# Optimization experiments

Measured on AMD Instinct MI355X. Metric: run time of the kernel, lower is better.

## Reference

```python
import jax, jax.numpy as jnp
import numpy as np

# Static sizes: S scenes of P pedestrians each; B = S*P total peds.
S, P, HD, ED, GH, GO, MD, T = 128, 32, 32, 16, 72, 8, 64, 8
B = S * P


def setup_inputs() -> dict:
    key = jax.random.key(0)
    ks = jax.random.split(key, 24)
    f32 = jnp.float32
    inp = {
        'last_pos': jax.random.normal(ks[0], (B, 2), f32),
        'last_pos_rel': jax.random.normal(ks[1], (B, 2), f32),
        'hh': jax.random.normal(ks[2], (B, HD), f32),
        'ch': jax.random.normal(ks[3], (B, HD), f32),
        # uniform scenes: [start, end) pairs
        'seq_start_end': jnp.stack([jnp.arange(S) * P, (jnp.arange(S) + 1) * P], axis=1).astype(jnp.int64),
        'end_group': jax.random.randint(ks[4], (B, 1), 0, 5, jnp.int32),
        # decoder spatial embedding Linear(2, ED)
        'W_se': jax.random.normal(ks[5], (2, ED), f32) * 0.5,
        'b_se': jax.random.normal(ks[6], (ED,), f32) * 0.05,
        # LSTM (num_layers=1), torch gate order i,f,g,o
        'Wih': jax.random.normal(ks[7], (4 * HD, ED), f32) * 0.15,
        'Whh': jax.random.normal(ks[8], (4 * HD, HD), f32) * 0.15,
        'bih': jax.random.normal(ks[9], (4 * HD,), f32) * 0.05,
        'bhh': jax.random.normal(ks[10], (4 * HD,), f32) * 0.05,
        # hidden2pos Linear(HD, 2)
        'W_hp': jax.random.normal(ks[11], (HD, 2), f32) * 0.15,
        'b_hp': jax.random.normal(ks[12], (2,), f32) * 0.05,
        # pooling spatial embedding Linear(2, ED)
        'W_pse': jax.random.normal(ks[13], (2, ED), f32) * 0.5,
        'b_pse': jax.random.normal(ks[14], (ED,), f32) * 0.05,
        # intra-group GCN weights (48->72->8)
        'W1a': jax.random.normal(ks[15], (ED + HD, GH), f32) * 0.05,
        'W2a': jax.random.normal(ks[16], (GH, GO), f32) * 0.05,
        # inter-group GCN weights
        'W1b': jax.random.normal(ks[17], (ED + HD, GH), f32) * 0.05,
        'W2b': jax.random.normal(ks[18], (GH, GO), f32) * 0.05,
        # mlp: (HD + 2*GO) -> MD -> HD, relu after each layer
        'W_m1': jax.random.normal(ks[19], (HD + 2 * GO, MD), f32) * 0.15,
        'b_m1': jax.random.normal(ks[20], (MD,), f32) * 0.05,
        'W_m2': jax.random.normal(ks[21], (MD, HD), f32) * 0.15,
        'b_m2': jax.random.normal(ks[22], (HD,), f32) * 0.05,
    }
    return inp


def _pool(h, pos, g, W_pse, b_pse, W1a, W2a, W1b, W2b):
    # h: [B,HD] hidden, pos: [B,2] current positions, g: [B] int group labels
    hid = h.reshape(S, P, HD)
    ps = pos.reshape(S, P, 2)
    gg = g.reshape(S, P)
    # rel[s,i,j] = pos[j] - pos[i]  (matches curr_end_pos_1 - curr_end_pos_2)
    rel = ps[:, None, :, :] - ps[:, :, None, :]
    emb = rel @ W_pse + b_pse                                     # [S,P,P,ED]
    X = jnp.concatenate([emb, jnp.broadcast_to(hid[:, None], (S, P, P, HD))], -1)
    e = jnp.eye(P, dtype=bool)
    # adj_all[i,j,k] = (j==k) | (i==j) | (i==k)
    adj_all = (e[None, :, :] | e[:, :, None] | e[:, None, :]).astype(X.dtype)
    same = ((gg[:, :, None] == gg[:, None, :]) & (gg[:, :, None] != 0)) | e[None]
    diff = (~same) | e[None]

    def norm(adj):
        # faithful to the original normalize(): divide adj[s,i,j,k] by sum_k adj[s,j,i,k]
        denom = jnp.sum(adj, axis=3)                               # [S,i,j]
        return adj / jnp.swapaxes(denom, 1, 2)[..., None]

    A_s = norm(adj_all[None] * same[:, None].astype(X.dtype))      # [S,P,P,P]
    A_d = norm(adj_all[None] * diff[:, None].astype(X.dtype))

    def gcn(A, H, W1, W2):
        H = jax.nn.relu(jnp.einsum('sijk,sikd->sijd', A, H) @ W1)
        H = jax.nn.relu(jnp.einsum('sijk,sikd->sijd', A, H) @ W2)
        return H

    feat = jnp.concatenate([gcn(A_s, X, W1a, W2a), gcn(A_d, X, W1b, W2b)], -1)  # [S,P,P,2*GO]
    return jnp.max(feat, axis=2).reshape(B, 2 * GO)


def reference(last_pos, last_pos_rel, hh, ch, seq_start_end, end_group,
              W_se, b_se, Wih, Whh, bih, bhh, W_hp, b_hp, W_pse, b_pse,
              W1a, W2a, W1b, W2b, W_m1, b_m1, W_m2, b_m2):
    g = end_group.reshape(-1)
    dec_in = last_pos_rel @ W_se + b_se

    def step(carry, _):
        h, c, lp, x = carry
        gates = x @ Wih.T + bih + h @ Whh.T + bhh
        i, f, gc, o = jnp.split(gates, 4, axis=-1)
        c2 = jax.nn.sigmoid(f) * c + jax.nn.sigmoid(i) * jnp.tanh(gc)
        h2 = jax.nn.sigmoid(o) * jnp.tanh(c2)
        rel_pos = h2 @ W_hp + b_hp
        cur = rel_pos + lp
        ph = _pool(h2, cur, g, W_pse, b_pse, W1a, W2a, W1b, W2b)
        dh = jax.nn.relu(jnp.concatenate([h2, ph], -1) @ W_m1 + b_m1)
        dh = jax.nn.relu(dh @ W_m2 + b_m2)
        x2 = rel_pos @ W_se + b_se
        return (dh, c2, cur, x2), rel_pos

    _, rels = jax.lax.scan(step, (hh, ch, last_pos, dec_in), None, length=T)
    return rels  # pred_traj_fake_rel: [T, B, 2]
```

## Files before the change

kernel.cpp:

```cpp
#include <hip/hip_runtime.h>

#define NS 128
#define NP 32
#define HD 32
#define ED 16
#define GH 72
#define GO 8
#define MD 64
#define TT 8
#define NB (NS*NP)
#define EW 76

#define SLOT 272
#define WS_NEED (256*2*SLOT*4)

typedef float v2f __attribute__((ext_vector_type(2)));

__device__ __forceinline__ float sigm(float x){ return 1.0f/(1.0f+__expf(-x)); }
__device__ __forceinline__ float tanhfast(float x){ return 1.0f - 2.0f/(__expf(2.0f*x)+1.0f); }
__device__ __forceinline__ unsigned rne16(float f){
  unsigned u = __float_as_uint(f);
  u += 0x7fffu + ((u>>16)&1u);
  return u>>16;
}
__device__ __forceinline__ float lo16(unsigned v){ return __uint_as_float(v<<16); }
__device__ __forceinline__ float hi16(unsigned v){ return __uint_as_float(v & 0xffff0000u); }
__device__ __forceinline__ float rdlane(float v, int l){
  return __int_as_float(__builtin_amdgcn_readlane(__float_as_int(v), l));
}
template<int C>
__device__ __forceinline__ float dppx(float x){
  return __int_as_float(__builtin_amdgcn_update_dpp(0, __float_as_int(x), C, 0xF, 0xF, true));
}
#define XOR1 0xB1
#define XOR2 0x4E

__global__ __launch_bounds__(1024, 1) void decoder_kernel_split(
    const float* __restrict__ last_pos, const float* __restrict__ last_pos_rel,
    const float* __restrict__ hh, const float* __restrict__ ch,
    const int*  __restrict__ eg,
    const float* __restrict__ W_se, const float* __restrict__ b_se,
    const float* __restrict__ Wih, const float* __restrict__ Whh,
    const float* __restrict__ bih, const float* __restrict__ bhh,
    const float* __restrict__ W_hp, const float* __restrict__ b_hp,
    const float* __restrict__ W_pse, const float* __restrict__ b_pse,
    const float* __restrict__ W1a, const float* __restrict__ W2a,
    const float* __restrict__ W1b, const float* __restrict__ W2b,
    const float* __restrict__ W_m1, const float* __restrict__ b_m1,
    const float* __restrict__ W_m2, const float* __restrict__ b_m2,
    float* __restrict__ out, float* __restrict__ ws)
{
  const int tid   = threadIdx.x;
  const int scn   = blockIdx.x >> 1;
  const int myM   = blockIdx.x & 1;
  const int lane  = tid & 31;
  const int grp32 = tid >> 5;

  __shared__ __align__(16) float uni[4096];
  __shared__ __align__(16) unsigned W1pT[GH][16];
  __shared__ __align__(16) float Wp1[2][GH];
  __shared__ __align__(16) float c1l[GH];
  __shared__ __align__(16) float ebuf[NP*EW];
  __shared__ __align__(16) float hbuf[NP][HD];
  __shared__ __align__(16) float h2buf[NP][36];
  __shared__ __align__(16) float GS[5][GH];
  __shared__ __align__(16) float phbuf[NP][16];
  __shared__ __align__(16) unsigned Wm1p[48][32];
  __shared__ __align__(16) unsigned Wm2p[32][32];
  __shared__ float lpbuf[NP][2], rpbuf[NP][2], Whp[HD][2];
  __shared__ float bm1l[MD], bm2l[HD], bhp2[2];
  __shared__ unsigned bm[NP];
  __shared__ unsigned gmsk[5];
  __shared__ float invn[NP];
  __shared__ int gl[NP];

  float* const a1 = uni;

  const int mybase = (scn*2 + myM)*2;
  const int pbase  = (scn*2 + 1 - myM)*2;

  const int myrow = tid & 127;
  const int pq4   = tid >> 7;
  float wrow[HD];
  #pragma unroll
  for (int c = 0; c < HD/4; c++) {
    float4 w = *(const float4*)(Whh + myrow*HD + c*4);
    wrow[c*4+0]=w.x; wrow[c*4+1]=w.y; wrow[c*4+2]=w.z; wrow[c*4+3]=w.w;
  }
  float wf0 = 0.f, wf1 = 0.f, bfr = bih[myrow] + bhh[myrow];
  #pragma unroll
  for (int e = 0; e < ED; e++) {
    float wv = Wih[myrow*ED + e];
    wf0 = fmaf(W_se[e],    wv, wf0);
    wf1 = fmaf(W_se[ED+e], wv, wf1);
    bfr = fmaf(b_se[e],    wv, bfr);
  }

  float creg = ch[(scn*NP + grp32)*HD + lane];
  hbuf[grp32][lane] = hh[(scn*NP + grp32)*HD + lane];

  if (tid < NP) {
    int gi = eg[scn*NP + tid];
    gl[tid] = gi;
    unsigned sm = 0;
    for (int j = 0; j < NP; j++) {
      int gj = eg[scn*NP + j];
      bool sj = (j == tid) || (gi == gj && gi != 0);
      sm |= ((unsigned)sj) << j;
    }
    unsigned mk = myM ? ((~sm) | (1u << tid)) : sm;
    bm[tid] = mk;
    invn[tid] = 1.0f/(float)__popc(mk);
  }
  if (tid < 5) {
    unsigned mv = 0;
    for (int j = 0; j < NP; j++) if (eg[scn*NP + j] == tid) mv |= (1u << j);
    gmsk[tid] = (tid == 0) ? 0xFFFFFFFFu : mv;
  }
  if (tid < 64) {
    int p = tid >> 1, k = tid & 1;
    lpbuf[p][k] = last_pos[(scn*NP+p)*2+k];
    rpbuf[p][k] = last_pos_rel[(scn*NP+p)*2+k];
    Whp[p][k]   = W_hp[tid];
    bm1l[tid]   = b_m1[tid];
  }
  if (tid < 32) bm2l[tid] = b_m2[tid];
  if (tid < 2)  bhp2[tid] = b_hp[tid];
  const float* W1my = myM ? W1b : W1a;
  const float* W2g  = myM ? W2b : W2a;
  if (tid < GH) {
    int d = tid;
    float s0 = 0.f, s1 = 0.f, sc1 = 0.f;
    for (int e = 0; e < ED; e++) {
      float w = W1my[e*GH + d];
      s0  += W_pse[e]    * w;
      s1  += W_pse[ED+e] * w;
      sc1 += b_pse[e]    * w;
    }
    Wp1[0][d] = s0; Wp1[1][d] = s1; c1l[d] = sc1;
  }
  #pragma unroll
  for (int r = 0; r < 2; r++) {
    int u = tid + 1024*r;
    if (u < 16*GH) {
      int k2 = u/GH, d = u%GH;
      unsigned lo = rne16(W1my[(ED+2*k2  )*GH + d]);
      unsigned hi = rne16(W1my[(ED+2*k2+1)*GH + d]);
      W1pT[d][k2] = lo | (hi << 16);
    }
  }
  #pragma unroll
  for (int r = 0; r < 2; r++) {
    int u = tid + 1024*r;
    if (u < 1536) {
      int k = u >> 5, uu = u & 31;
      Wm1p[k][uu] = rne16(W_m1[k*MD + uu]) | (rne16(W_m1[k*MD + 32 + uu]) << 16);
    }
  }
  {
    int k = tid >> 5, uu = tid & 31;
    Wm2p[k][uu] = rne16(W_m2[k*HD + uu]) | (rne16(W_m2[(k+32)*HD + uu]) << 16);
  }
  __syncthreads();

  for (int t = 0; t < TT; t++) {
    {
      float hv[4];
      #pragma unroll
      for (int pp2 = 0; pp2 < 4; pp2++) hv[pp2] = hbuf[pq4*4 + pp2][lane];
      float rG[4];
      #pragma unroll
      for (int pp2 = 0; pp2 < 4; pp2++) {
        int p = pq4*4 + pp2;
        float acc = fmaf(rpbuf[p][0], wf0, fmaf(rpbuf[p][1], wf1, bfr));
        #pragma unroll
        for (int c = 0; c < HD; c++)
          acc = fmaf(rdlane(hv[pp2], c), wrow[c], acc);
        rG[pp2] = acc;
      }
      #pragma unroll
      for (int pp2 = 0; pp2 < 4; pp2++) uni[(pq4*4+pp2)*128 + myrow] = rG[pp2];
    }
    __syncthreads();

    {
      int p = grp32, n = lane;
      float gi_ = uni[p*128 +       n];
      float gf_ = uni[p*128 +  32 + n];
      float gg_ = uni[p*128 +  64 + n];
      float go_ = uni[p*128 +  96 + n];
      float c2 = sigm(gf_)*creg + sigm(gi_)*tanhfast(gg_);
      creg = c2;
      float h2 = sigm(go_)*tanhfast(c2);
      h2buf[p][n] = h2;
      float r0 = h2 * Whp[n][0];
      float r1 = h2 * Whp[n][1];
      r0 += dppx<XOR1>(r0); r1 += dppx<XOR1>(r1);
      r0 += dppx<XOR2>(r0); r1 += dppx<XOR2>(r1);
      #pragma unroll
      for (int off = 4; off < 32; off <<= 1) {
        r0 += __shfl_xor(r0, off, 32);
        r1 += __shfl_xor(r1, off, 32);
      }
      r0 += bhp2[0]; r1 += bhp2[1];
      if (n == 0) {
        if (myM == 0) {
          out[t*NB*2 + (scn*NP+p)*2 + 0] = r0;
          out[t*NB*2 + (scn*NP+p)*2 + 1] = r1;
        }
        rpbuf[p][0] = r0;  rpbuf[p][1] = r1;
        lpbuf[p][0] += r0; lpbuf[p][1] += r1;
      }
    }
    __syncthreads();

    {
      const int j = lane;
      float lpj0 = lpbuf[j][0], lpj1 = lpbuf[j][1];
      float h2row[HD];
      #pragma unroll
      for (int c = 0; c < 8; c++) {
        float4 v = *(const float4*)&h2buf[j][c*4];
        h2row[c*4+0]=v.x; h2row[c*4+1]=v.y; h2row[c*4+2]=v.z; h2row[c*4+3]=v.w;
      }
      #pragma unroll
      for (int r = 0; r < 3; r++) {
        int d = grp32 + 32*r;
        if (d < GH) {
          float av = fmaf(lpj0, Wp1[0][d], lpj1*Wp1[1][d]);
          #pragma unroll
          for (int k8 = 0; k8 < 4; k8++) {
            uint4 w4 = *(const uint4*)&W1pT[d][k8*4];
            av = fmaf(h2row[k8*8+0], lo16(w4.x), av);
            av = fmaf(h2row[k8*8+1], hi16(w4.x), av);
            av = fmaf(h2row[k8*8+2], lo16(w4.y), av);
            av = fmaf(h2row[k8*8+3], hi16(w4.y), av);
            av = fmaf(h2row[k8*8+4], lo16(w4.z), av);
            av = fmaf(h2row[k8*8+5], hi16(w4.z), av);
            av = fmaf(h2row[k8*8+6], lo16(w4.w), av);
            av = fmaf(h2row[k8*8+7], hi16(w4.w), av);
          }
          a1[j*EW + d] = av;
        }
      }
      #pragma unroll
      for (int ii = 0; ii < 3; ii++) {
        int idx = tid + 1024*ii;
        if (idx < NP*GH) {
          int d = idx >> 5, i2 = idx & 31;
          ebuf[i2*EW + d] = fmaf(-lpbuf[i2][1], Wp1[1][d],
                            fmaf(-lpbuf[i2][0], Wp1[0][d], c1l[d]));
        }
      }
    }
    __syncthreads();

    if (tid < 5*GH) {
      int g = tid / GH, d = tid - g*GH;
      unsigned gmv = gmsk[g];
      float tot = 0.f, sg = 0.f;
      #pragma unroll
      for (int j2 = 0; j2 < NP; j2++) {
        float av = a1[j2*EW + d];
        tot += av;
        sg  += ((gmv >> j2) & 1u) ? av : 0.f;
      }
      GS[g][d] = myM ? ((g == 0) ? tot : tot - sg)
                     : ((g == 0) ? tot : sg);
    }
    __syncthreads();

    {
      const int j = lane, i = grp32;
      unsigned bmv = bm[i];
      bool mij = (bmv >> j) & 1u;
      bool diag = (j == i);
      int gi = gl[i];
      float in_ = invn[i];
      const float *p0, *p1; float c0, c1c;
      if (diag) {
        if (myM == 0) { p0 = gi ? &GS[gi][0] : (a1 + i*EW); c0 = in_; p1 = a1 + i*EW; c1c = 0.f; }
        else          { p0 = &GS[gi][0];                    c0 = in_; p1 = a1 + i*EW; c1c = gi ? in_ : 0.f; }
      } else if (mij) { p0 = a1 + j*EW; c0 = 0.5f; p1 = a1 + i*EW; c1c = 0.5f; }
      else            { p0 = a1 + j*EW; c0 = 1.0f; p1 = a1 + j*EW; c1c = 0.f; }
      const float* erow = ebuf + i*EW;
      v2f qv[4];
      #pragma unroll
      for (int h = 0; h < 4; h++) qv[h] = (v2f){0.f, 0.f};
      for (int d4 = 0; d4 < GH/4; d4++) {
        float4 e4 = *(const float4*)(erow + d4*4);
        float4 va = diag ? *(const float4*)(p0 + d4*4)
                         : *(const float4*)(a1 + j*EW + d4*4);
        float4 vb = *(const float4*)(p1 + d4*4);
        float tv[4];
        tv[0] = fmaxf(fmaf(c0, va.x, fmaf(c1c, vb.x, e4.x)), 0.f);
        tv[1] = fmaxf(fmaf(c0, va.y, fmaf(c1c, vb.y, e4.y)), 0.f);
        tv[2] = fmaxf(fmaf(c0, va.z, fmaf(c1c, vb.z, e4.z)), 0.f);
        tv[3] = fmaxf(fmaf(c0, va.w, fmaf(c1c, vb.w, e4.w)), 0.f);
        #pragma unroll
        for (int k = 0; k < 4; k++) {
          const float* wr = W2g + (d4*4+k)*GO;
          v2f wA = {wr[0], wr[1]}, wB = {wr[2], wr[3]};
          v2f wC = {wr[4], wr[5]}, wD = {wr[6], wr[7]};
          v2f tk = {tv[k], tv[k]};
          qv[0] += tk*wA; qv[1] += tk*wB; qv[2] += tk*wC; qv[3] += tk*wD;
        }
      }
      float q[8];
      #pragma unroll
      for (int h = 0; h < 4; h++) { q[2*h] = qv[h][0]; q[2*h+1] = qv[h][1]; }
      float sq[8];
      #pragma unroll
      for (int o = 0; o < 8; o++) sq[o] = mij ? q[o] : 0.f;
      #pragma unroll
      for (int o = 0; o < 8; o++) sq[o] += dppx<XOR1>(sq[o]);
      #pragma unroll
      for (int o = 0; o < 8; o++) sq[o] += dppx<XOR2>(sq[o]);
      #pragma unroll
      for (int off = 4; off < 32; off <<= 1) {
        #pragma unroll
        for (int o = 0; o < 8; o++) sq[o] += __shfl_xor(sq[o], off, 32);
      }
      float qd[8];
      #pragma unroll
      for (int o = 0; o < 8; o++) qd[o] = __shfl(q[o], i, 32);
      float F[8];
      if (diag) {
        #pragma unroll
        for (int o = 0; o < 8; o++) F[o] = fmaxf(sq[o]*in_, 0.f);
      } else {
        float scl = mij ? 0.5f : 1.0f;
        #pragma unroll
        for (int o = 0; o < 8; o++)
          F[o] = fmaxf((q[o] + (mij ? qd[o] : 0.f))*scl, 0.f);
      }
      #pragma unroll
      for (int o = 0; o < 8; o++) F[o] = fmaxf(F[o], dppx<XOR1>(F[o]));
      #pragma unroll
      for (int o = 0; o < 8; o++) F[o] = fmaxf(F[o], dppx<XOR2>(F[o]));
      #pragma unroll
      for (int off = 4; off < 32; off <<= 1) {
        #pragma unroll
        for (int o = 0; o < 8; o++) F[o] = fmaxf(F[o], __shfl_xor(F[o], off, 32));
      }
      if (j == 0) {
        const int slw = (mybase + (t & 1))*SLOT;
        #pragma unroll
        for (int o = 0; o < 8; o++) {
          phbuf[i][myM*GO + o] = F[o];
          atomicExch(ws + slw + i*8 + o, F[o]);
        }
      }
    }
    __syncthreads();

    const int sl  = (mybase + (t & 1))*SLOT;
    const int psl = (pbase  + (t & 1))*SLOT;
    if (tid == 0) atomicExch((unsigned*)(ws + sl + 256), (unsigned)(t + 1));
    asm volatile("" ::: "memory");
    const int p4 = grp32, u4 = lane;
    float m1lo = bm1l[u4], m1hi = bm1l[32 + u4];
    {
      #pragma unroll
      for (int c = 0; c < 8; c++) {
        float4 v = *(const float4*)&h2buf[p4][c*4];
        unsigned w0 = Wm1p[c*4+0][u4], w1 = Wm1p[c*4+1][u4];
        unsigned w2 = Wm1p[c*4+2][u4], w3 = Wm1p[c*4+3][u4];
        m1lo = fmaf(v.x, lo16(w0), m1lo); m1hi = fmaf(v.x, hi16(w0), m1hi);
        m1lo = fmaf(v.y, lo16(w1), m1lo); m1hi = fmaf(v.y, hi16(w1), m1hi);
        m1lo = fmaf(v.z, lo16(w2), m1lo); m1hi = fmaf(v.z, hi16(w2), m1hi);
        m1lo = fmaf(v.w, lo16(w3), m1lo); m1hi = fmaf(v.w, hi16(w3), m1hi);
      }
    }
    asm volatile("" ::: "memory");
    if (tid == 0) {
      while (atomicAdd((unsigned*)(ws + psl + 256), 0u) != (unsigned)(t + 1))
        __builtin_amdgcn_s_sleep(2);
    }
    __syncthreads();
    if (tid < 256) {
      int p = tid >> 3, o = tid & 7;
      phbuf[p][(1-myM)*8 + o] = atomicAdd(ws + psl + tid, 0.0f);
    }
    __syncthreads();

    {
      float4 f0 = *(const float4*)&phbuf[p4][0];
      float4 f1 = *(const float4*)&phbuf[p4][4];
      float4 f2 = *(const float4*)&phbuf[p4][8];
      float4 f3 = *(const float4*)&phbuf[p4][12];
      float pv[16] = {f0.x,f0.y,f0.z,f0.w, f1.x,f1.y,f1.z,f1.w,
                      f2.x,f2.y,f2.z,f2.w, f3.x,f3.y,f3.z,f3.w};
      #pragma unroll
      for (int k = 0; k < 16; k++) {
        unsigned v = Wm1p[32 + k][u4];
        m1lo = fmaf(pv[k], lo16(v), m1lo);
        m1hi = fmaf(pv[k], hi16(v), m1hi);
      }
      m1lo = fmaxf(m1lo, 0.f); m1hi = fmaxf(m1hi, 0.f);
      float* mb = uni + 2048 + p4*64;
      mb[u4]      = m1lo;
      mb[32 + u4] = m1hi;
      float acc = bm2l[u4];
      #pragma unroll
      for (int k4 = 0; k4 < 8; k4++) {
        float4 lo4 = *(const float4*)(mb + k4*4);
        float4 hi4 = *(const float4*)(mb + 32 + k4*4);
        unsigned v0 = Wm2p[k4*4+0][u4], v1 = Wm2p[k4*4+1][u4];
        unsigned v2 = Wm2p[k4*4+2][u4], v3 = Wm2p[k4*4+3][u4];
        acc = fmaf(lo4.x, lo16(v0), acc); acc = fmaf(hi4.x, hi16(v0), acc);
        acc = fmaf(lo4.y, lo16(v1), acc); acc = fmaf(hi4.y, hi16(v1), acc);
        acc = fmaf(lo4.z, lo16(v2), acc); acc = fmaf(hi4.z, hi16(v2), acc);
        acc = fmaf(lo4.w, lo16(v3), acc); acc = fmaf(hi4.w, hi16(v3), acc);
      }
      hbuf[p4][u4] = fmaxf(acc, 0.f);
    }
    __syncthreads();
  }
}

__global__ __launch_bounds__(1024, 1) void decoder_kernel_mono(
    const float* __restrict__ last_pos, const float* __restrict__ last_pos_rel,
    const float* __restrict__ hh, const float* __restrict__ ch,
    const int*  __restrict__ eg,
    const float* __restrict__ W_se, const float* __restrict__ b_se,
    const float* __restrict__ Wih, const float* __restrict__ Whh,
    const float* __restrict__ bih, const float* __restrict__ bhh,
    const float* __restrict__ W_hp, const float* __restrict__ b_hp,
    const float* __restrict__ W_pse, const float* __restrict__ b_pse,
    const float* __restrict__ W1a, const float* __restrict__ W2a,
    const float* __restrict__ W1b, const float* __restrict__ W2b,
    const float* __restrict__ W_m1, const float* __restrict__ b_m1,
    const float* __restrict__ W_m2, const float* __restrict__ b_m2,
    float* __restrict__ out)
{
  const int tid   = threadIdx.x;
  const int scn   = blockIdx.x;
  const int lane  = tid & 31;
  const int grp32 = tid >> 5;

  __shared__ __align__(16) float uni[4864];
  __shared__ __align__(16) unsigned W1p[2][16][GH];
  __shared__ __align__(16) float W2l[2][GH][GO];
  __shared__ __align__(16) float Wp1[2][2][GH];
  __shared__ __align__(16) float c1l[2][GH];
  __shared__ __align__(16) float hbuf[NP][HD];
  __shared__ __align__(16) float h2buf[NP][36];
  __shared__ __align__(16) float GS[2][5][GH];
  __shared__ __align__(16) float phbuf[NP][16];
  __shared__ __align__(16) unsigned Wm1p[48][32];
  __shared__ __align__(16) unsigned Wm2p[32][32];
  __shared__ float lpbuf[NP][2], rpbuf[NP][2], Whp[HD][2];
  __shared__ float bm1l[MD], bm2l[HD], bhp2[2];
  __shared__ unsigned bm[2][NP];
  __shared__ float invn[2][NP];
  __shared__ int gl[NP];

  const int myrow = tid & 127;
  const int pq4   = tid >> 7;
  float wrow[HD];
  #pragma unroll
  for (int c = 0; c < HD/4; c++) {
    float4 w = *(const float4*)(Whh + myrow*HD + c*4);
    wrow[c*4+0]=w.x; wrow[c*4+1]=w.y; wrow[c*4+2]=w.z; wrow[c*4+3]=w.w;
  }
  float wf0 = 0.f, wf1 = 0.f, bfr = bih[myrow] + bhh[myrow];
  #pragma unroll
  for (int e = 0; e < ED; e++) {
    float wv = Wih[myrow*ED + e];
    wf0 = fmaf(W_se[e],    wv, wf0);
    wf1 = fmaf(W_se[ED+e], wv, wf1);
    bfr = fmaf(b_se[e],    wv, bfr);
  }
  float creg = ch[(scn*NP + grp32)*HD + lane];
  hbuf[grp32][lane] = hh[(scn*NP + grp32)*HD + lane];

  if (tid < NP) {
    int gi = eg[scn*NP + tid];
    gl[tid] = gi;
    unsigned sm = 0;
    for (int j = 0; j < NP; j++) {
      int gj = eg[scn*NP + j];
      bool sj = (j == tid) || (gi == gj && gi != 0);
      sm |= ((unsigned)sj) << j;
    }
    unsigned dm = (~sm) | (1u << tid);
    bm[0][tid] = sm; bm[1][tid] = dm;
    invn[0][tid] = 1.0f/(float)__popc(sm);
    invn[1][tid] = 1.0f/(float)__popc(dm);
  }
  if (tid < 64) {
    int p = tid >> 1, k = tid & 1;
    lpbuf[p][k] = last_pos[(scn*NP+p)*2+k];
    rpbuf[p][k] = last_pos_rel[(scn*NP+p)*2+k];
    Whp[p][k]   = W_hp[tid];
    bm1l[tid]   = b_m1[tid];
  }
  if (tid < 32) bm2l[tid] = b_m2[tid];
  if (tid < 2)  bhp2[tid] = b_hp[tid];
  if (tid < 2*GH) {
    int m = tid / GH, d = tid % GH;
    const float* W1 = m ? W1b : W1a;
    float s0 = 0.f, s1 = 0.f, sc1 = 0.f;
    for (int e = 0; e < ED; e++) {
      float w = W1[e*GH + d];
      s0 += W_pse[e]*w; s1 += W_pse[ED+e]*w; sc1 += b_pse[e]*w;
    }
    Wp1[m][0][d] = s0; Wp1[m][1][d] = s1; c1l[m][d] = sc1;
  }
  {
    int u = tid;
    if (u < 2*GH*GO) {
      int m = u/(GH*GO), rest = u%(GH*GO);
      W2l[m][rest/GO][rest%GO] = (m ? W2b : W2a)[rest];
    }
    if (tid < 128) {
      int u2 = tid + 1024;
      int m = u2/(GH*GO), rest = u2%(GH*GO);
      W2l[m][rest/GO][rest%GO] = (m ? W2b : W2a)[rest];
    }
  }
  #pragma unroll
  for (int r = 0; r < 3; r++) {
    int u = tid + 1024*r;
    if (u < 2304) {
      int m = u/1152, rest = u%1152, k2 = rest/GH, d = rest%GH;
      const float* W1 = m ? W1b : W1a;
      W1p[m][k2][d] = rne16(W1[(ED+2*k2)*GH + d]) | (rne16(W1[(ED+2*k2+1)*GH + d]) << 16);
    }
  }
  #pragma unroll
  for (int r = 0; r < 2; r++) {
    int u = tid + 1024*r;
    if (u < 1536) {
      int k = u >> 5, uu = u & 31;
      Wm1p[k][uu] = rne16(W_m1[k*MD + uu]) | (rne16(W_m1[k*MD + 32 + uu]) << 16);
    }
  }
  {
    int k = tid >> 5, uu = tid & 31;
    Wm2p[k][uu] = rne16(W_m2[k*HD + uu]) | (rne16(W_m2[(k+32)*HD + uu]) << 16);
  }
  __syncthreads();

  for (int t = 0; t < TT; t++) {
    {
      float rG[4];
      #pragma unroll
      for (int pp2 = 0; pp2 < 4; pp2++) {
        int p = pq4*4 + pp2;
        float acc = fmaf(rpbuf[p][0], wf0, fmaf(rpbuf[p][1], wf1, bfr));
        #pragma unroll
        for (int c = 0; c < 8; c++) {
          float4 h4 = *(const float4*)&hbuf[p][c*4];
          acc = fmaf(h4.x, wrow[c*4+0], acc);
          acc = fmaf(h4.y, wrow[c*4+1], acc);
          acc = fmaf(h4.z, wrow[c*4+2], acc);
          acc = fmaf(h4.w, wrow[c*4+3], acc);
        }
        rG[pp2] = acc;
      }
      #pragma unroll
      for (int pp2 = 0; pp2 < 4; pp2++) uni[(pq4*4+pp2)*128 + myrow] = rG[pp2];
    }
    __syncthreads();
    {
      int p = grp32, n = lane;
      float gi_ = uni[p*128 + n];
      float gf_ = uni[p*128 + 32 + n];
      float gg_ = uni[p*128 + 64 + n];
      float go_ = uni[p*128 + 96 + n];
      float c2 = sigm(gf_)*creg + sigm(gi_)*tanhfast(gg_);
      creg = c2;
      float h2 = sigm(go_)*tanhfast(c2);
      h2buf[p][n] = h2;
      float r0 = h2 * Whp[n][0];
      float r1 = h2 * Whp[n][1];
      #pragma unroll
      for (int off = 1; off < 32; off <<= 1) {
        r0 += __shfl_xor(r0, off, 32);
        r1 += __shfl_xor(r1, off, 32);
      }
      r0 += bhp2[0]; r1 += bhp2[1];
      if (n == 0) {
        out[t*NB*2 + (scn*NP+p)*2 + 0] = r0;
        out[t*NB*2 + (scn*NP+p)*2 + 1] = r1;
        rpbuf[p][0] = r0;  rpbuf[p][1] = r1;
        lpbuf[p][0] += r0; lpbuf[p][1] += r1;
      }
    }
    __syncthreads();
    {
      const int j = lane;
      float lpj0 = lpbuf[j][0], lpj1 = lpbuf[j][1];
      float h2row[HD];
      #pragma unroll
      for (int c = 0; c < 8; c++) {
        float4 v = *(const float4*)&h2buf[j][c*4];
        h2row[c*4+0]=v.x; h2row[c*4+1]=v.y; h2row[c*4+2]=v.z; h2row[c*4+3]=v.w;
      }
      #pragma unroll
      for (int r = 0; r < 5; r++) {
        int rest = grp32 + 32*r;
        if (rest < 144) {
          int m = rest >= 72 ? 1 : 0;
          int d = rest - 72*m;
          float pp_ = fmaf(lpj0, Wp1[m][0][d], lpj1*Wp1[m][1][d]);
          float av = pp_;
          #pragma unroll
          for (int k2 = 0; k2 < 16; k2++) {
            unsigned v = W1p[m][k2][d];
            av = fmaf(h2row[2*k2], lo16(v), av);
            av = fmaf(h2row[2*k2+1], hi16(v), av);
          }
          uni[m*2432 + j*76 + d] = av;
          int gj = gl[j];
          float tot = av;
          float s1 = (gj==1)?av:0.f, s2=(gj==2)?av:0.f, s3=(gj==3)?av:0.f, s4=(gj==4)?av:0.f;
          #pragma unroll
          for (int off = 1; off < 32; off <<= 1) {
            tot += __shfl_xor(tot, off, 32);
            s1 += __shfl_xor(s1, off, 32);
            s2 += __shfl_xor(s2, off, 32);
            s3 += __shfl_xor(s3, off, 32);
            s4 += __shfl_xor(s4, off, 32);
          }
          if (j < 5) {
            float v2;
            if (m == 0) v2 = (j==0)?tot:((j==1)?s1:((j==2)?s2:((j==3)?s3:s4)));
            else        v2 = (j==0)?tot:((j==1)?tot-s1:((j==2)?tot-s2:((j==3)?tot-s3:tot-s4)));
            GS[m][j][d] = v2;
          }
        }
      }
    }
    __syncthreads();
    {
      const int j   = lane;
      const int m   = tid >> 9;
      const int sub = (tid >> 5) & 15;
      const float* am = uni + m*2432;
      int   I2[2] = {sub, sub + 16};
      const float *P0[2], *P1[2];
      float C0[2], C1[2], NL0[2], NL1[2];
      bool  MIJ[2], DIAG[2];
      v2f qv[2][4];
      #pragma unroll
      for (int r = 0; r < 2; r++) {
        int i = I2[r];
        unsigned bmv = bm[m][i];
        bool mij = (bmv >> j) & 1u;
        bool diag = (j == i);
        int gi = gl[i];
        float in_ = invn[m][i];
        const float *p0, *p1; float c0, c1c;
        if (diag) {
          if (m == 0) { p0 = gi ? &GS[0][gi][0] : (am + i*76); c0 = in_; p1 = am + i*76; c1c = 0.f; }
          else        { p0 = &GS[1][gi][0];                    c0 = in_; p1 = am + i*76; c1c = gi ? in_ : 0.f; }
        } else if (mij) { p0 = am + j*76; c0 = 0.5f; p1 = am + i*76; c1c = 0.5f; }
        else            { p0 = am + j*76; c0 = 1.0f; p1 = am + j*76; c1c = 0.f; }
        P0[r]=p0; P1[r]=p1; C0[r]=c0; C1[r]=c1c; MIJ[r]=mij; DIAG[r]=diag;
        NL0[r] = -lpbuf[i][0]; NL1[r] = -lpbuf[i][1];
        #pragma unroll
        for (int h = 0; h < 4; h++) qv[r][h] = (v2f){0.f, 0.f};
      }
      for (int d4 = 0; d4 < GH/4; d4++) {
        float4 c14 = *(const float4*)&c1l[m][d4*4];
        float4 w04 = *(const float4*)&Wp1[m][0][d4*4];
        float4 w14 = *(const float4*)&Wp1[m][1][d4*4];
        float4 vaS = *(const float4*)(am + j*76 + d4*4);
        float4 va0 = vaS, va1 = vaS;
        if (DIAG[0]) va0 = *(const float4*)(P0[0] + d4*4);
        if (DIAG[1]) va1 = *(const float4*)(P0[1] + d4*4);
        float4 vb0 = *(const float4*)(P1[0] + d4*4);
        float4 vb1 = *(const float4*)(P1[1] + d4*4);
        float e0x = fmaf(NL1[0], w14.x, fmaf(NL0[0], w04.x, c14.x));
        float e0y = fmaf(NL1[0], w14.y, fmaf(NL0[0], w04.y, c14.y));
        float e0z = fmaf(NL1[0], w14.z, fmaf(NL0[0], w04.z, c14.z));
        float e0w = fmaf(NL1[0], w14.w, fmaf(NL0[0], w04.w, c14.w));
        float e1x = fmaf(NL1[1], w14.x, fmaf(NL0[1], w04.x, c14.x));
        float e1y = fmaf(NL1[1], w14.y, fmaf(NL0[1], w04.y, c14.y));
        float e1z = fmaf(NL1[1], w14.z, fmaf(NL0[1], w04.z, c14.z));
        float e1w = fmaf(NL1[1], w14.w, fmaf(NL0[1], w04.w, c14.w));
        float tv0[4], tv1[4];
        tv0[0] = fmaxf(fmaf(C0[0], va0.x, fmaf(C1[0], vb0.x, e0x)), 0.f);
        tv0[1] = fmaxf(fmaf(C0[0], va0.y, fmaf(C1[0], vb0.y, e0y)), 0.f);
        tv0[2] = fmaxf(fmaf(C0[0], va0.z, fmaf(C1[0], vb0.z, e0z)), 0.f);
        tv0[3] = fmaxf(fmaf(C0[0], va0.w, fmaf(C1[0], vb0.w, e0w)), 0.f);
        tv1[0] = fmaxf(fmaf(C0[1], va1.x, fmaf(C1[1], vb1.x, e1x)), 0.f);
        tv1[1] = fmaxf(fmaf(C0[1], va1.y, fmaf(C1[1], vb1.y, e1y)), 0.f);
        tv1[2] = fmaxf(fmaf(C0[1], va1.z, fmaf(C1[1], vb1.z, e1z)), 0.f);
        tv1[3] = fmaxf(fmaf(C0[1], va1.w, fmaf(C1[1], vb1.w, e1w)), 0.f);
        #pragma unroll
        for (int k = 0; k < 4; k++) {
          const v2f* w2p = (const v2f*)&W2l[m][d4*4+k][0];
          v2f wA = w2p[0], wB = w2p[1], wC = w2p[2], wD = w2p[3];
          v2f t0 = {tv0[k], tv0[k]};
          qv[0][0] += t0*wA; qv[0][1] += t0*wB; qv[0][2] += t0*wC; qv[0][3] += t0*wD;
          v2f t1 = {tv1[k], tv1[k]};
          qv[1][0] += t1*wA; qv[1][1] += t1*wB; qv[1][2] += t1*wC; qv[1][3] += t1*wD;
        }
      }
      #pragma unroll
      for (int r = 0; r < 2; r++) {
        float q[8];
        #pragma unroll
        for (int h = 0; h < 4; h++) { q[2*h] = qv[r][h][0]; q[2*h+1] = qv[r][h][1]; }
        float sq[8];
        #pragma unroll
        for (int o = 0; o < 8; o++) sq[o] = MIJ[r] ? q[o] : 0.f;
        #pragma unroll
        for (int off = 1; off < 32; off <<= 1) {
          #pragma unroll
          for (int o = 0; o < 8; o++) sq[o] += __shfl_xor(sq[o], off, 32);
        }
        float qd[8];
        #pragma unroll
        for (int o = 0; o < 8; o++) qd[o] = __shfl(q[o], I2[r], 32);
        float in_ = invn[m][I2[r]];
        float F[8];
        if (DIAG[r]) {
          #pragma unroll
          for (int o = 0; o < 8; o++) F[o] = fmaxf(sq[o]*in_, 0.f);
        } else {
          float scl = MIJ[r] ? 0.5f : 1.0f;
          #pragma unroll
          for (int o = 0; o < 8; o++)
            F[o] = fmaxf((q[o] + (MIJ[r] ? qd[o] : 0.f))*scl, 0.f);
        }
        #pragma unroll
        for (int off = 1; off < 32; off <<= 1) {
          #pragma unroll
          for (int o = 0; o < 8; o++) F[o] = fmaxf(F[o], __shfl_xor(F[o], off, 32));
        }
        if (j == 0) {
          #pragma unroll
          for (int o = 0; o < 8; o++) phbuf[I2[r]][m*GO + o] = F[o];
        }
      }
    }
    __syncthreads();
    {
      int p = grp32, u = lane;
      float in48[48];
      #pragma unroll
      for (int c = 0; c < 8; c++) {
        float4 v = *(const float4*)&h2buf[p][c*4];
        in48[c*4+0]=v.x; in48[c*4+1]=v.y; in48[c*4+2]=v.z; in48[c*4+3]=v.w;
      }
      #pragma unroll
      for (int c = 0; c < 4; c++) {
        float4 v = *(const float4*)&phbuf[p][c*4];
        in48[32+c*4+0]=v.x; in48[32+c*4+1]=v.y; in48[32+c*4+2]=v.z; in48[32+c*4+3]=v.w;
      }
      float m1lo = bm1l[u], m1hi = bm1l[32 + u];
      #pragma unroll
      for (int k = 0; k < 48; k++) {
        unsigned v = Wm1p[k][u];
        m1lo = fmaf(in48[k], lo16(v), m1lo);
        m1hi = fmaf(in48[k], hi16(v), m1hi);
      }
      m1lo = fmaxf(m1lo, 0.f); m1hi = fmaxf(m1hi, 0.f);
      float acc = bm2l[u];
      #pragma unroll
      for (int k = 0; k < 32; k++) {
        unsigned v = Wm2p[k][u];
        acc = fmaf(__shfl(m1lo, k, 32), lo16(v), acc);
        acc = fmaf(__shfl(m1hi, k, 32), hi16(v), acc);
      }
      hbuf[p][u] = fmaxf(acc, 0.f);
    }
    __syncthreads();
  }
}

extern "C" void kernel_launch(void* const* d_in, const int* in_sizes, int n_in,
                              void* d_out, int out_size, void* d_ws, size_t ws_size,
                              hipStream_t stream) {
  (void)in_sizes; (void)n_in; (void)out_size;
  const float* last_pos     = (const float*)d_in[0];
  const float* last_pos_rel = (const float*)d_in[1];
  const float* hh           = (const float*)d_in[2];
  const float* ch           = (const float*)d_in[3];
  const int*  eg            = (const int*) d_in[5];
  const float* W_se  = (const float*)d_in[6];
  const float* b_se  = (const float*)d_in[7];
  const float* Wih   = (const float*)d_in[8];
  const float* Whh   = (const float*)d_in[9];
  const float* bih   = (const float*)d_in[10];
  const float* bhh   = (const float*)d_in[11];
  const float* W_hp  = (const float*)d_in[12];
  const float* b_hp  = (const float*)d_in[13];
  const float* W_pse = (const float*)d_in[14];
  const float* b_pse = (const float*)d_in[15];
  const float* W1a   = (const float*)d_in[16];
  const float* W2a   = (const float*)d_in[17];
  const float* W1b   = (const float*)d_in[18];
  const float* W2b   = (const float*)d_in[19];
  const float* W_m1  = (const float*)d_in[20];
  const float* b_m1  = (const float*)d_in[21];
  const float* W_m2  = (const float*)d_in[22];
  const float* b_m2  = (const float*)d_in[23];
  float* out = (float*)d_out;

  if (ws_size >= (size_t)WS_NEED) {
    decoder_kernel_split<<<2*NS, 1024, 0, stream>>>(
        last_pos, last_pos_rel, hh, ch, eg,
        W_se, b_se, Wih, Whh, bih, bhh, W_hp, b_hp, W_pse, b_pse,
        W1a, W2a, W1b, W2b, W_m1, b_m1, W_m2, b_m2, out, (float*)d_ws);
  } else {
    decoder_kernel_mono<<<NS, 1024, 0, stream>>>(
        last_pos, last_pos_rel, hh, ch, eg,
        W_se, b_se, Wih, Whh, bih, bhh, W_hp, b_hp, W_pse, b_pse,
        W1a, W2a, W1b, W2b, W_m1, b_m1, W_m2, b_m2, out);
  }
}
```

Before: 248.2 us.

## Transpose MLP weights, swizzle h2 buffer, and remap blocks to scene pairs

Stores the packed bf16 MLP weights transposed per output unit so each lane reads a uint4 instead of four scalar LDS loads. The h2 buffer uses an XOR-style rotated layout to avoid bank conflicts on row-wise float4 reads. The LSTM recurrent matvec reads h from LDS as float4 broadcasts instead of 32 readlane ops. The blockIdx mapping of scenes to the paired split blocks also changes, so the two halves of a scene land on different block indices, which may affect where they are scheduled. Costs are extra LDS padding and changed access patterns whose conflict behaviour is not guaranteed.

Result: slower. 288.1 us (+16.0%).

```diff
diff --git a/kernel.cpp b/kernel.cpp
--- a/kernel.cpp
+++ b/kernel.cpp
@@ -14,6 +14,8 @@
 #define SLOT 272
 #define WS_NEED (256*2*SLOT*4)
 
+#define H2G(row,c) (((row)<<5) + (((((c)-(row)))&7)<<2))
+
 typedef float v2f __attribute__((ext_vector_type(2)));
 
 __device__ __forceinline__ float sigm(float x){ return 1.0f/(1.0f+__expf(-x)); }
@@ -25,9 +27,6 @@
 }
 __device__ __forceinline__ float lo16(unsigned v){ return __uint_as_float(v<<16); }
 __device__ __forceinline__ float hi16(unsigned v){ return __uint_as_float(v & 0xffff0000u); }
-__device__ __forceinline__ float rdlane(float v, int l){
-  return __int_as_float(__builtin_amdgcn_readlane(__float_as_int(v), l));
-}
 template<int C>
 __device__ __forceinline__ float dppx(float x){
   return __int_as_float(__builtin_amdgcn_update_dpp(0, __float_as_int(x), C, 0xF, 0xF, true));
@@ -51,8 +50,9 @@
     float* __restrict__ out, float* __restrict__ ws)
 {
   const int tid   = threadIdx.x;
-  const int scn   = blockIdx.x >> 1;
-  const int myM   = blockIdx.x & 1;
+  const int bid   = blockIdx.x;
+  const int scn   = (bid & 7) | ((bid >> 4) << 3);
+  const int myM   = (bid >> 3) & 1;
   const int lane  = tid & 31;
   const int grp32 = tid >> 5;
 
@@ -62,11 +62,11 @@
   __shared__ __align__(16) float c1l[GH];
   __shared__ __align__(16) float ebuf[NP*EW];
   __shared__ __align__(16) float hbuf[NP][HD];
-  __shared__ __align__(16) float h2buf[NP][36];
+  __shared__ __align__(16) float h2s[NP*32];
   __shared__ __align__(16) float GS[5][GH];
   __shared__ __align__(16) float phbuf[NP][16];
-  __shared__ __align__(16) unsigned Wm1p[48][32];
-  __shared__ __align__(16) unsigned Wm2p[32][32];
+  __shared__ __align__(16) unsigned WmT1[NP][52];
+  __shared__ __align__(16) unsigned WmT2[NP][36];
   __shared__ float lpbuf[NP][2], rpbuf[NP][2], Whp[HD][2];
   __shared__ float bm1l[MD], bm2l[HD], bhp2[2];
   __shared__ unsigned bm[NP];
@@ -151,31 +151,33 @@
   }
   #pragma unroll
   for (int r = 0; r < 2; r++) {
-    int u = tid + 1024*r;
-    if (u < 1536) {
-      int k = u >> 5, uu = u & 31;
-      Wm1p[k][uu] = rne16(W_m1[k*MD + uu]) | (rne16(W_m1[k*MD + 32 + uu]) << 16);
+    int idx = tid + 1024*r;
+    if (idx < 48*NP) {
+      int k = idx >> 5, u = idx & 31;
+      WmT1[u][k] = rne16(W_m1[k*MD + u]) | (rne16(W_m1[k*MD + 32 + u]) << 16);
     }
   }
   {
-    int k = tid >> 5, uu = tid & 31;
-    Wm2p[k][uu] = rne16(W_m2[k*HD + uu]) | (rne16(W_m2[(k+32)*HD + uu]) << 16);
+    int k = tid >> 5, u = tid & 31;
+    WmT2[u][k] = rne16(W_m2[k*HD + u]) | (rne16(W_m2[(k+32)*HD + u]) << 16);
   }
   __syncthreads();
 
   for (int t = 0; t < TT; t++) {
     {
-      float hv[4];
-      #pragma unroll
-      for (int pp2 = 0; pp2 < 4; pp2++) hv[pp2] = hbuf[pq4*4 + pp2][lane];
       float rG[4];
       #pragma unroll
       for (int pp2 = 0; pp2 < 4; pp2++) {
         int p = pq4*4 + pp2;
         float acc = fmaf(rpbuf[p][0], wf0, fmaf(rpbuf[p][1], wf1, bfr));
         #pragma unroll
-        for (int c = 0; c < HD; c++)
-          acc = fmaf(rdlane(hv[pp2], c), wrow[c], acc);
+        for (int c = 0; c < 8; c++) {
+          float4 h4 = *(const float4*)&hbuf[p][c*4];
+          acc = fmaf(h4.x, wrow[c*4+0], acc);
+          acc = fmaf(h4.y, wrow[c*4+1], acc);
+          acc = fmaf(h4.z, wrow[c*4+2], acc);
+          acc = fmaf(h4.w, wrow[c*4+3], acc);
+        }
         rG[pp2] = acc;
       }
       #pragma unroll
@@ -192,7 +194,7 @@
       float c2 = sigm(gf_)*creg + sigm(gi_)*tanhfast(gg_);
       creg = c2;
       float h2 = sigm(go_)*tanhfast(c2);
-      h2buf[p][n] = h2;
+      h2s[H2G(p, n>>2) + (n&3)] = h2;
       float r0 = h2 * Whp[n][0];
       float r1 = h2 * Whp[n][1];
       r0 += dppx<XOR1>(r0); r1 += dppx<XOR1>(r1);
@@ -220,7 +222,7 @@
       float h2row[HD];
       #pragma unroll
       for (int c = 0; c < 8; c++) {
-        float4 v = *(const float4*)&h2buf[j][c*4];
+        float4 v = *(const float4*)&h2s[H2G(j, c)];
         h2row[c*4+0]=v.x; h2row[c*4+1]=v.y; h2row[c*4+2]=v.z; h2row[c*4+3]=v.w;
       }
       #pragma unroll
@@ -359,17 +361,17 @@
     if (tid == 0) atomicExch((unsigned*)(ws + sl + 256), (unsigned)(t + 1));
     asm volatile("" ::: "memory");
     const int p4 = grp32, u4 = lane;
+    const unsigned* wrow1 = &WmT1[u4][0];
     float m1lo = bm1l[u4], m1hi = bm1l[32 + u4];
     {
       #pragma unroll
       for (int c = 0; c < 8; c++) {
-        float4 v = *(const float4*)&h2buf[p4][c*4];
-        unsigned w0 = Wm1p[c*4+0][u4], w1 = Wm1p[c*4+1][u4];
-        unsigned w2 = Wm1p[c*4+2][u4], w3 = Wm1p[c*4+3][u4];
-        m1lo = fmaf(v.x, lo16(w0), m1lo); m1hi = fmaf(v.x, hi16(w0), m1hi);
-        m1lo = fmaf(v.y, lo16(w1), m1lo); m1hi = fmaf(v.y, hi16(w1), m1hi);
-        m1lo = fmaf(v.z, lo16(w2), m1lo); m1hi = fmaf(v.z, hi16(w2), m1hi);
-        m1lo = fmaf(v.w, lo16(w3), m1lo); m1hi = fmaf(v.w, hi16(w3), m1hi);
+        float4 v = *(const float4*)&h2s[H2G(p4, c)];
+        uint4 w = *(const uint4*)(wrow1 + c*4);
+        m1lo = fmaf(v.x, lo16(w.x), m1lo); m1hi = fmaf(v.x, hi16(w.x), m1hi);
+        m1lo = fmaf(v.y, lo16(w.y), m1lo); m1hi = fmaf(v.y, hi16(w.y), m1hi);
+        m1lo = fmaf(v.z, lo16(w.z), m1lo); m1hi = fmaf(v.z, hi16(w.z), m1hi);
+        m1lo = fmaf(v.w, lo16(w.w), m1lo); m1hi = fmaf(v.w, hi16(w.w), m1hi);
       }
     }
     asm volatile("" ::: "memory");
@@ -385,17 +387,14 @@
     __syncthreads();
 
     {
-      float4 f0 = *(const float4*)&phbuf[p4][0];
-      float4 f1 = *(const float4*)&phbuf[p4][4];
-      float4 f2 = *(const float4*)&phbuf[p4][8];
-      float4 f3 = *(const float4*)&phbuf[p4][12];
-      float pv[16] = {f0.x,f0.y,f0.z,f0.w, f1.x,f1.y,f1.z,f1.w,
-                      f2.x,f2.y,f2.z,f2.w, f3.x,f3.y,f3.z,f3.w};
-      #pragma unroll
-      for (int k = 0; k < 16; k++) {
-        unsigned v = Wm1p[32 + k][u4];
-        m1lo = fmaf(pv[k], lo16(v), m1lo);
-        m1hi = fmaf(pv[k], hi16(v), m1hi);
+      #pragma unroll
+      for (int c = 0; c < 4; c++) {
+        float4 f = *(const float4*)&phbuf[p4][c*4];
+        uint4 w = *(const uint4*)(wrow1 + 32 + c*4);
+        m1lo = fmaf(f.x, lo16(w.x), m1lo); m1hi = fmaf(f.x, hi16(w.x), m1hi);
+        m1lo = fmaf(f.y, lo16(w.y), m1lo); m1hi = fmaf(f.y, hi16(w.y), m1hi);
+        m1lo = fmaf(f.z, lo16(w.z), m1lo); m1hi = fmaf(f.z, hi16(w.z), m1hi);
+        m1lo = fmaf(f.w, lo16(w.w), m1lo); m1hi = fmaf(f.w, hi16(w.w), m1hi);
       }
       m1lo = fmaxf(m1lo, 0.f); m1hi = fmaxf(m1hi, 0.f);
       float* mb = uni + 2048 + p4*64;
@@ -406,12 +405,11 @@
       for (int k4 = 0; k4 < 8; k4++) {
         float4 lo4 = *(const float4*)(mb + k4*4);
         float4 hi4 = *(const float4*)(mb + 32 + k4*4);
-        unsigned v0 = Wm2p[k4*4+0][u4], v1 = Wm2p[k4*4+1][u4];
-        unsigned v2 = Wm2p[k4*4+2][u4], v3 = Wm2p[k4*4+3][u4];
-        acc = fmaf(lo4.x, lo16(v0), acc); acc = fmaf(hi4.x, hi16(v0), acc);
-        acc = fmaf(lo4.y, lo16(v1), acc); acc = fmaf(hi4.y, hi16(v1), acc);
-        acc = fmaf(lo4.z, lo16(v2), acc); acc = fmaf(hi4.z, hi16(v2), acc);
-        acc = fmaf(lo4.w, lo16(v3), acc); acc = fmaf(hi4.w, hi16(v3), acc);
+        uint4 w = *(const uint4*)(&WmT2[u4][k4*4]);
+        acc = fmaf(lo4.x, lo16(w.x), acc); acc = fmaf(hi4.x, hi16(w.x), acc);
+        acc = fmaf(lo4.y, lo16(w.y), acc); acc = fmaf(hi4.y, hi16(w.y), acc);
+        acc = fmaf(lo4.z, lo16(w.z), acc); acc = fmaf(hi4.z, hi16(w.z), acc);
+        acc = fmaf(lo4.w, lo16(w.w), acc); acc = fmaf(hi4.w, hi16(w.w), acc);
       }
       hbuf[p4][u4] = fmaxf(acc, 0.f);
     }
```
